# Kernel tuning notes

Measured on AMD Instinct MI355X. Metric: run time of the kernel, lower is better.

The kernel has to match this reference:

```python
import jax, jax.numpy as jnp
import numpy as np

DEPTH = 10
NUM_LEAVES = 2 ** DEPTH  # 1024


def setup_inputs() -> dict:
    key = jax.random.key(0)
    k1, k2, k3, k4 = jax.random.split(key, 4)
    B, C, T = 4096, 512, 4096
    x = jax.random.normal(k1, (B, C), dtype=jnp.float32)
    # thresholds = 6*rand - 3, as in __init__
    thresholds = 6.0 * jax.random.uniform(k2, (T, NUM_LEAVES - 1), dtype=jnp.float32) - 3.0
    ordinals = jax.random.randint(k3, (T, NUM_LEAVES - 1), 0, C, dtype=jnp.int32)
    weights = jax.random.normal(k4, (T, NUM_LEAVES), dtype=jnp.float32)
    return {"x": x, "thresholds": thresholds, "ordinals": ordinals, "weights": weights}


def reference(x, thresholds, ordinals, weights):
    """Random hinge forest forward.

    For each sample b and tree t: traverse the perfect binary tree of depth
    DEPTH.  At node n, margin m = x[b, ordinals[t, n]] - thresholds[t, n];
    go right (child 2n+2) if m > 0 else left (child 2n+1).  Track the signed
    margin of minimum magnitude along the path.  Output is
    |min-margin| * weights[t, leaf].
    """
    B = x.shape[0]
    T = thresholds.shape[0]
    tr = jnp.arange(T)  # [T], broadcasts against [B, T] node indices
    node = jnp.zeros((B, T), dtype=jnp.int32)
    minm = jnp.full((B, T), jnp.inf, dtype=x.dtype)
    for _ in range(DEPTH):
        thr = thresholds[tr, node]                      # [B, T]
        ordv = ordinals[tr, node]                       # [B, T] feature ids
        feat = jnp.take_along_axis(x, ordv, axis=1)     # [B, T]
        m = feat - thr
        minm = jnp.where(jnp.abs(m) < jnp.abs(minm), m, minm)
        node = 2 * node + 1 + (m > 0).astype(jnp.int32)
    leaf = node - (NUM_LEAVES - 1)                      # [B, T] in [0, 2^depth)
    w = weights[tr, leaf]                               # [B, T]
    return jnp.abs(minm) * w
```

## Files before the change

kernel.cpp:

```cpp
#include <hip/hip_runtime.h>
#include <hip/hip_fp16.h>

#define BB 4096
#define CC 512
#define TT 4096
#define NN 1023
#define NL 1024


__device__ __forceinline__ unsigned pack_node(float th, int o) {
    return ((unsigned)o << 16) | (unsigned)__half_as_ushort(__float2half(th));
}

__global__ __launch_bounds__(256)
void pack_trees(const float* __restrict__ thr, const int* __restrict__ ord,
                const float* __restrict__ wts, unsigned* __restrict__ pk_lo,
                uint2* __restrict__ p8, uint4* __restrict__ tails) {
    int t = blockIdx.x, tid = threadIdx.x;
    const float* tr = thr + (size_t)t * NN;
    const int*   oo = ord + (size_t)t * NN;
    unsigned* plo = pk_lo + ((size_t)t << 8);
    plo[tid] = (tid == 0) ? 0u : pack_node(tr[tid - 1], oo[tid - 1]);
    if (tid < 128) {
        int j = tid;
        p8[((size_t)t << 7) + j] =
            make_uint2(pack_node(tr[255 + 2 * j], oo[255 + 2 * j]),
                       pack_node(tr[256 + 2 * j], oo[256 + 2 * j]));
    }
    int i = tid;
    int nL = 511 + 2 * i, nR = 512 + 2 * i;
    unsigned ndL = pack_node(tr[nL], oo[nL]);
    unsigned ndR = pack_node(tr[nR], oo[nR]);
    float4 w4 = *(const float4*)(wts + ((size_t)t << 10) + 4 * i);
    unsigned w01 = (unsigned)__half_as_ushort(__float2half(w4.x)) |
                   ((unsigned)__half_as_ushort(__float2half(w4.y)) << 16);
    unsigned w23 = (unsigned)__half_as_ushort(__float2half(w4.z)) |
                   ((unsigned)__half_as_ushort(__float2half(w4.w)) << 16);
    tails[((size_t)t << 8) + i] = make_uint4(ndL, ndR, w01, w23);
}

__global__ __launch_bounds__(256)
void pack_x16(const float* __restrict__ x, unsigned short* __restrict__ xt16) {
    __shared__ float tile[64][65];
    int tx = threadIdx.x & 63, ty = threadIdx.x >> 6;
    int b0 = blockIdx.x * 64;
    int c0 = blockIdx.y * 64;
    #pragma unroll
    for (int i = 0; i < 16; ++i) {
        int rr = i * 4 + ty;
        tile[rr][tx] = x[(size_t)(b0 + rr) * CC + c0 + tx];
    }
    __syncthreads();
    #pragma unroll
    for (int i = 0; i < 16; ++i) {
        int cr = i * 4 + ty;
        xt16[(size_t)(c0 + cr) * BB + b0 + tx] =
            __half_as_ushort(__float2half(tile[tx][cr]));
    }
}

typedef unsigned short u16x2 __attribute__((ext_vector_type(2)));

static __device__ __forceinline__ unsigned psub_f16x2(unsigned a, unsigned b) {
    __half2 ah, bh;
    __builtin_memcpy(&ah, &a, 4);
    __builtin_memcpy(&bh, &b, 4);
    __half2 r = ah - bh;
    unsigned u; __builtin_memcpy(&u, &r, 4); return u;
}
static __device__ __forceinline__ unsigned pmin_u16x2(unsigned a, unsigned b) {
    u16x2 av, bv;
    __builtin_memcpy(&av, &a, 4);
    __builtin_memcpy(&bv, &b, 4);
    u16x2 m = __builtin_elementwise_min(av, bv);
    unsigned u; __builtin_memcpy(&u, &m, 4); return u;
}
static __device__ __forceinline__ float f16lo(unsigned u) {
    return __half2float(__ushort_as_half((unsigned short)(u & 0xffffu)));
}
static __device__ __forceinline__ float f16hi(unsigned u) {
    return __half2float(__ushort_as_half((unsigned short)(u >> 16)));
}

#define LDS_BYTES 163840

typedef __attribute__((address_space(1))) const void gv_t;
typedef __attribute__((address_space(3))) void lv_t;

__global__ __launch_bounds__(1024, 1)
void rhf_main(const unsigned* __restrict__ pk_lo, const uint2* __restrict__ p8g,
              const uint4* __restrict__ tails, const unsigned short* __restrict__ xt16,
              float* __restrict__ out) {
    extern __shared__ char smem[];
    unsigned short* xs16 = (unsigned short*)smem;
    unsigned*       trl  = (unsigned*)(smem + 65536);
    float*          res  = (float*)(smem + 131072);

    const int tid  = threadIdx.x;
    const int lane = tid & 63;
    const int wv   = tid >> 6;
    const int bi   = blockIdx.x;
    const int tb    = ((bi & 7) << 2) + ((bi >> 3) >> 6);
    const int panel = (bi >> 3) & 63;

    const char* gsrc0 = (const char*)pk_lo + ((size_t)(tb * 128) << 10);
    char* ldst = (char*)trl + wv * 4096 + lane * 16;
    auto dma = [&](int g) {
        const char* s = gsrc0 + ((size_t)(g * 64 + wv * 4) << 10) + lane * 16;
        #pragma unroll
        for (int q = 0; q < 4; ++q)
            __builtin_amdgcn_global_load_lds((gv_t*)(s + q * 1024),
                                             (lv_t*)(ldst + q * 1024), 16, 0, 0);
    };

    dma(0);

    {
        const unsigned short* src = xt16 + (size_t)panel * 64;
        #pragma unroll
        for (int k = 0; k < 4; ++k) {
            int i4 = k * 1024 + tid;
            int c  = i4 >> 3;
            int o8 = (i4 & 7) << 3;
            uint4 v = *(const uint4*)(src + (size_t)c * BB + o8);
            *(uint4*)(xs16 + ((size_t)i4 << 3)) = v;
        }
    }
    __syncthreads();

    auto evalpair = [&](unsigned nd_a, unsigned nd_b, unsigned& amin,
                        unsigned& r_a, unsigned& r_b) {
        unsigned thv2 = (nd_a & 0xffffu) | (nd_b << 16);
        unsigned short fa = xs16[((nd_a >> 16) << 6) + lane];
        unsigned short fb = xs16[((nd_b >> 16) << 6) + lane];
        unsigned feat2 = (unsigned)fa | ((unsigned)fb << 16);
        unsigned mb = psub_f16x2(feat2, thv2);
        amin = pmin_u16x2(amin, mb & 0x7fff7fffu);
        r_a = ((mb >> 15) & 1u) ^ 1u;
        r_b = (mb >> 31) ^ 1u;
    };

    #pragma unroll 1
    for (int g = 0; g < 2; ++g) {
        if (g > 0) {
            asm volatile("s_waitcnt vmcnt(0)" ::: "memory");
            __builtin_amdgcn_sched_barrier(0);
        }
        const int t0 = tb * 128 + g * 64 + wv * 4;
        const unsigned* pkw = trl + wv * 1024;

        unsigned amin01 = 0x7c007c00u, amin23 = 0x7c007c00u;
        int sl0 = 1, sl1 = 1, sl2 = 1, sl3 = 1;
        unsigned nd0 = pkw[1], nd1 = pkw[256 + 1], nd2 = pkw[512 + 1], nd3 = pkw[768 + 1];

        #pragma unroll
        for (int d = 0; d < 7; ++d) {
            uint2 ch0 = *(const uint2*)(pkw +       2 * sl0);
            uint2 ch1 = *(const uint2*)(pkw + 256 + 2 * sl1);
            uint2 ch2 = *(const uint2*)(pkw + 512 + 2 * sl2);
            uint2 ch3 = *(const uint2*)(pkw + 768 + 2 * sl3);
            unsigned r0, r1, r2, r3;
            evalpair(nd0, nd1, amin01, r0, r1);
            evalpair(nd2, nd3, amin23, r2, r3);
            sl0 = 2 * sl0 + (int)r0; nd0 = r0 ? ch0.y : ch0.x;
            sl1 = 2 * sl1 + (int)r1; nd1 = r1 ? ch1.y : ch1.x;
            sl2 = 2 * sl2 + (int)r2; nd2 = r2 ? ch2.y : ch2.x;
            sl3 = 2 * sl3 + (int)r3; nd3 = r3 ? ch3.y : ch3.x;
        }

        const uint2* p8t = p8g + ((size_t)t0 << 7);
        uint2 q0 = p8t[        sl0 - 128];
        uint2 q1 = p8t[128 +   sl1 - 128];
        uint2 q2 = p8t[256 +   sl2 - 128];
        uint2 q3 = p8t[384 +   sl3 - 128];
        {
            unsigned r0, r1, r2, r3;
            evalpair(nd0, nd1, amin01, r0, r1);
            evalpair(nd2, nd3, amin23, r2, r3);
            sl0 = 2 * sl0 + (int)r0; nd0 = r0 ? q0.y : q0.x;
            sl1 = 2 * sl1 + (int)r1; nd1 = r1 ? q1.y : q1.x;
            sl2 = 2 * sl2 + (int)r2; nd2 = r2 ? q2.y : q2.x;
            sl3 = 2 * sl3 + (int)r3; nd3 = r3 ? q3.y : q3.x;
        }

        const uint4* tt = tails + ((size_t)t0 << 8);
        uint4 e0 = tt[        sl0 - 256];
        uint4 e1 = tt[256 +   sl1 - 256];
        uint4 e2 = tt[512 +   sl2 - 256];
        uint4 e3 = tt[768 +   sl3 - 256];
        if (g == 0) { dma(1); __builtin_amdgcn_sched_barrier(0); }
        unsigned w0, w1, w2, w3;
        {
            unsigned r0, r1, r2, r3;
            evalpair(nd0, nd1, amin01, r0, r1);
            evalpair(nd2, nd3, amin23, r2, r3);
            nd0 = r0 ? e0.y : e0.x;  w0 = r0 ? e0.w : e0.z;
            nd1 = r1 ? e1.y : e1.x;  w1 = r1 ? e1.w : e1.z;
            nd2 = r2 ? e2.y : e2.x;  w2 = r2 ? e2.w : e2.z;
            nd3 = r3 ? e3.y : e3.x;  w3 = r3 ? e3.w : e3.z;
        }

        {
            unsigned r0, r1, r2, r3;
            evalpair(nd0, nd1, amin01, r0, r1);
            evalpair(nd2, nd3, amin23, r2, r3);
            unsigned short wb0 = (unsigned short)(r0 ? (w0 >> 16) : (w0 & 0xffffu));
            unsigned short wb1 = (unsigned short)(r1 ? (w1 >> 16) : (w1 & 0xffffu));
            unsigned short wb2 = (unsigned short)(r2 ? (w2 >> 16) : (w2 & 0xffffu));
            unsigned short wb3 = (unsigned short)(r3 ? (w3 >> 16) : (w3 & 0xffffu));
            float o0 = f16lo(amin01) * __half2float(__ushort_as_half(wb0));
            float o1 = f16hi(amin01) * __half2float(__ushort_as_half(wb1));
            float o2 = f16lo(amin23) * __half2float(__ushort_as_half(wb2));
            float o3 = f16hi(amin23) * __half2float(__ushort_as_half(wb3));
            int col0 = g * 64 + wv * 4;
            res[(lane << 7) + ((col0 +     lane) & 127)] = o0;
            res[(lane << 7) + ((col0 + 1 + lane) & 127)] = o1;
            res[(lane << 7) + ((col0 + 2 + lane) & 127)] = o2;
            res[(lane << 7) + ((col0 + 3 + lane) & 127)] = o3;
        }
    }
    __syncthreads();

    float* obase = out + (size_t)(tb * 128);
    #pragma unroll
    for (int k = 0; k < 8; ++k) {
        int idx = k * 1024 + tid;
        int rr = idx >> 7, cc = idx & 127;
        float v = res[(rr << 7) + ((cc + rr) & 127)];
        obase[((size_t)panel * 64 + rr) * TT + cc] = v;
    }
}

#define F_SP 32
#define F_TG 16
#define F_GROUPS 8
#define F_TPB (F_TG * F_GROUPS)
#define F_NPANELS (BB / F_SP)
#define F_LDS 147456

__global__ __launch_bounds__(512, 1)
void rhf_fallback(const float* __restrict__ x, const float* __restrict__ thr_g,
                  const int* __restrict__ ord_g, const float* __restrict__ wts,
                  float* __restrict__ out) {
    extern __shared__ char smem[];
    float*        xs  = (float*)(smem);
    unsigned int* pk  = (unsigned int*)(smem + 65536);
    float*        res = (float*)(smem + 131072);
    const int tid = threadIdx.x, s = tid & 31, slot = tid >> 5;
    const int panel = blockIdx.x & (F_NPANELS - 1), tb = blockIdx.x >> 7;
    const float* xbase = x + (size_t)panel * F_SP * CC;
    #pragma unroll
    for (int k = 0; k < (F_SP * CC) / 512; ++k) {
        int idx = k * 512 + tid, r = idx >> 9, c = idx & 511;
        xs[(c << 5) + r] = xbase[r * CC + c];
    }
    float4 pthr[8]; int4 pord[8]; float tthr[3]; int tord[3];
    auto prefetch = [&](int g) {
        const size_t base = (size_t)(tb * F_TPB + g * F_TG + slot) * NN;
        #pragma unroll
        for (int k = 0; k < 8; ++k) {
            int j = k * 128 + 4 * s;
            if (j < 1020) { pthr[k] = *(const float4*)(thr_g + base + j);
                            pord[k] = *(const int4*)(ord_g + base + j); }
            else { tthr[0]=thr_g[base+1020]; tord[0]=ord_g[base+1020];
                   tthr[1]=thr_g[base+1021]; tord[1]=ord_g[base+1021];
                   tthr[2]=thr_g[base+1022]; tord[2]=ord_g[base+1022]; }
        }
    };
    auto pack1 = [](float f, int o) -> unsigned int {
        return ((unsigned int)o << 16) | (unsigned int)__half_as_ushort(__float2half(f));
    };
    auto commit = [&]() {
        unsigned int* pt = pk + (slot << 10);
        #pragma unroll
        for (int k = 0; k < 8; ++k) {
            int j = k * 128 + 4 * s;
            if (j < 1020) {
                pt[1+j+0]=pack1(pthr[k].x,pord[k].x); pt[1+j+1]=pack1(pthr[k].y,pord[k].y);
                pt[1+j+2]=pack1(pthr[k].z,pord[k].z); pt[1+j+3]=pack1(pthr[k].w,pord[k].w);
            } else { pt[1+1020]=pack1(tthr[0],tord[0]); pt[1+1021]=pack1(tthr[1],tord[1]);
                     pt[1+1022]=pack1(tthr[2],tord[2]); }
        }
    };
    prefetch(0);
    __builtin_amdgcn_sched_barrier(0);
    for (int g = 0; g < F_GROUPS; ++g) {
        __syncthreads();
        commit();
        __syncthreads();
        if (g + 1 < F_GROUPS) prefetch(g + 1);
        __builtin_amdgcn_sched_barrier(0);
        const int t = tb * F_TPB + g * F_TG + slot;
        const unsigned int* pkt = pk + (slot << 10);
        float minm = __builtin_inff();
        int sl = 1;
        unsigned int cur = pkt[1];
        #pragma unroll
        for (int d = 0; d < 10; ++d) {
            uint2 ch;
            if (d < 9) ch = *(const uint2*)(pkt + 2 * sl);
            float thv = __half2float(__ushort_as_half((unsigned short)(cur & 0xffffu)));
            int orv = (int)(cur >> 16);
            float feat = xs[(orv << 5) + s];
            float m = feat - thv;
            bool take = fabsf(m) < fabsf(minm);
            minm = take ? m : minm;
            int right = (m > 0.0f) ? 1 : 0;
            sl = 2 * sl + right;
            if (d < 9) cur = right ? ch.y : ch.x;
        }
        int leaf = sl - NL;
        float w = wts[(size_t)t * NL + leaf];
        int col = g * F_TG + slot;
        res[(s << 7) + ((col + s) & 127)] = fabsf(minm) * w;
    }
    __syncthreads();
    float* obase = out + (size_t)panel * F_SP * TT + (size_t)tb * F_TPB;
    #pragma unroll
    for (int k = 0; k < (F_SP * F_TPB) / 512; ++k) {
        int idx = k * 512 + tid, rr = idx >> 7, c = idx & 127;
        obase[(size_t)rr * TT + c] = res[(rr << 7) + ((c + rr) & 127)];
    }
}

extern "C" void kernel_launch(void* const* d_in, const int* in_sizes, int n_in,
                              void* d_out, int out_size, void* d_ws, size_t ws_size,
                              hipStream_t stream) {
    const float* x    = (const float*)d_in[0];
    const float* thr  = (const float*)d_in[1];
    const int*   ordv = (const int*)d_in[2];
    const float* wts  = (const float*)d_in[3];
    float*       out  = (float*)d_out;

    const size_t pk_bytes   = (size_t)TT * 256 * 4;
    const size_t p8_bytes   = (size_t)TT * 128 * 8;
    const size_t tail_bytes = (size_t)TT * 256 * 16;
    const size_t xt_bytes   = (size_t)CC * BB * 2;

    if (d_ws && ws_size >= pk_bytes + p8_bytes + tail_bytes + xt_bytes) {
        unsigned*       pk_lo = (unsigned*)d_ws;
        uint2*          p8    = (uint2*)((char*)d_ws + pk_bytes);
        uint4*          tails = (uint4*)((char*)d_ws + pk_bytes + p8_bytes);
        unsigned short* xt16  = (unsigned short*)((char*)d_ws + pk_bytes + p8_bytes + tail_bytes);
        pack_trees<<<TT, 256, 0, stream>>>(thr, ordv, wts, pk_lo, p8, tails);
        dim3 gx(BB / 64, CC / 64);
        pack_x16<<<gx, 256, 0, stream>>>(x, xt16);
        (void)hipFuncSetAttribute((const void*)rhf_main,
                            hipFuncAttributeMaxDynamicSharedMemorySize, LDS_BYTES);
        rhf_main<<<2048, 1024, LDS_BYTES, stream>>>(pk_lo, p8, tails, xt16, out);
    } else {
        (void)hipFuncSetAttribute((const void*)rhf_fallback,
                            hipFuncAttributeMaxDynamicSharedMemorySize, F_LDS);
        rhf_fallback<<<F_NPANELS * (TT / F_TPB), 512, F_LDS, stream>>>(x, thr, ordv, wts, out);
    }
}
```

Baseline: 114.6 us.

## Stage only top seven tree levels in LDS and interleave eight trees per wave

Only the first 7 levels of each tree (128 nodes) are now staged in LDS, so all 128 trees of a block fit in one load and the two-pass loop with its mid-kernel DMA disappears. Level 7 moves to a new global g7 array. Each wave now traverses 8 trees at once instead of 4, giving more independent loads in flight. The ordinal is pre-shifted by 23 so it becomes a byte offset into the x tile, removing a shift per lookup. In exchange, one more dependent global gather is added per sample, and register pressure rises with the wider interleave.

```diff
diff --git a/kernel.cpp b/kernel.cpp
--- a/kernel.cpp
+++ b/kernel.cpp
@@ -9,21 +9,30 @@
 
 
 __device__ __forceinline__ unsigned pack_node(float th, int o) {
-    return ((unsigned)o << 16) | (unsigned)__half_as_ushort(__float2half(th));
+    return ((unsigned)o << 23) | (unsigned)__half_as_ushort(__float2half(th));
 }
 
 __global__ __launch_bounds__(256)
 void pack_trees(const float* __restrict__ thr, const int* __restrict__ ord,
                 const float* __restrict__ wts, unsigned* __restrict__ pk_lo,
-                uint2* __restrict__ p8, uint4* __restrict__ tails) {
+                uint2* __restrict__ g7, uint2* __restrict__ g8,
+                uint4* __restrict__ tails) {
     int t = blockIdx.x, tid = threadIdx.x;
     const float* tr = thr + (size_t)t * NN;
     const int*   oo = ord + (size_t)t * NN;
-    unsigned* plo = pk_lo + ((size_t)t << 8);
-    plo[tid] = (tid == 0) ? 0u : pack_node(tr[tid - 1], oo[tid - 1]);
+    if (tid < 128) {
+        unsigned* plo = pk_lo + ((size_t)t << 7);
+        plo[tid] = (tid == 0) ? 0u : pack_node(tr[tid - 1], oo[tid - 1]);
+    }
+    if (tid < 64) {
+        int j = tid;
+        g7[((size_t)t << 6) + j] =
+            make_uint2(pack_node(tr[127 + 2 * j], oo[127 + 2 * j]),
+                       pack_node(tr[128 + 2 * j], oo[128 + 2 * j]));
+    }
     if (tid < 128) {
         int j = tid;
-        p8[((size_t)t << 7) + j] =
+        g8[((size_t)t << 7) + j] =
             make_uint2(pack_node(tr[255 + 2 * j], oo[255 + 2 * j]),
                        pack_node(tr[256 + 2 * j], oo[256 + 2 * j]));
     }
@@ -88,13 +97,13 @@
 typedef __attribute__((address_space(3))) void lv_t;
 
 __global__ __launch_bounds__(1024, 1)
-void rhf_main(const unsigned* __restrict__ pk_lo, const uint2* __restrict__ p8g,
-              const uint4* __restrict__ tails, const unsigned short* __restrict__ xt16,
-              float* __restrict__ out) {
+void rhf_main(const unsigned* __restrict__ pk_lo, const uint2* __restrict__ g7g,
+              const uint2* __restrict__ g8g, const uint4* __restrict__ tails,
+              const unsigned short* __restrict__ xt16, float* __restrict__ out) {
     extern __shared__ char smem[];
-    unsigned short* xs16 = (unsigned short*)smem;
-    unsigned*       trl  = (unsigned*)(smem + 65536);
-    float*          res  = (float*)(smem + 131072);
+    const char*     xsb = (const char*)smem;
+    unsigned*       trl = (unsigned*)(smem + 65536);
+    float*          res = (float*)(smem + 131072);
 
     const int tid  = threadIdx.x;
     const int lane = tid & 63;
@@ -102,18 +111,16 @@
     const int bi   = blockIdx.x;
     const int tb    = ((bi & 7) << 2) + ((bi >> 3) >> 6);
     const int panel = (bi >> 3) & 63;
-
-    const char* gsrc0 = (const char*)pk_lo + ((size_t)(tb * 128) << 10);
-    char* ldst = (char*)trl + wv * 4096 + lane * 16;
-    auto dma = [&](int g) {
-        const char* s = gsrc0 + ((size_t)(g * 64 + wv * 4) << 10) + lane * 16;
+    const int lane2 = lane << 1;
+
+    {
+        const char* s = (const char*)pk_lo + ((size_t)(tb * 128 + wv * 8) << 9) + lane * 16;
+        char* d = (char*)trl + wv * 4096 + lane * 16;
         #pragma unroll
         for (int q = 0; q < 4; ++q)
             __builtin_amdgcn_global_load_lds((gv_t*)(s + q * 1024),
-                                             (lv_t*)(ldst + q * 1024), 16, 0, 0);
-    };
-
-    dma(0);
+                                             (lv_t*)(d + q * 1024), 16, 0, 0);
+    }
 
     {
         const unsigned short* src = xt16 + (size_t)panel * 64;
@@ -123,16 +130,19 @@
             int c  = i4 >> 3;
             int o8 = (i4 & 7) << 3;
             uint4 v = *(const uint4*)(src + (size_t)c * BB + o8);
-            *(uint4*)(xs16 + ((size_t)i4 << 3)) = v;
+            *(uint4*)((char*)smem + ((size_t)i4 << 4)) = v;
         }
     }
     __syncthreads();
+
+    const int t0 = tb * 128 + wv * 8;
+    const unsigned* pkw = trl + wv * 1024;
 
     auto evalpair = [&](unsigned nd_a, unsigned nd_b, unsigned& amin,
                         unsigned& r_a, unsigned& r_b) {
         unsigned thv2 = (nd_a & 0xffffu) | (nd_b << 16);
-        unsigned short fa = xs16[((nd_a >> 16) << 6) + lane];
-        unsigned short fb = xs16[((nd_b >> 16) << 6) + lane];
+        unsigned short fa = *(const unsigned short*)(xsb + (nd_a >> 16) + lane2);
+        unsigned short fb = *(const unsigned short*)(xsb + (nd_b >> 16) + lane2);
         unsigned feat2 = (unsigned)fa | ((unsigned)fb << 16);
         unsigned mb = psub_f16x2(feat2, thv2);
         amin = pmin_u16x2(amin, mb & 0x7fff7fffu);
@@ -140,83 +150,88 @@
         r_b = (mb >> 31) ^ 1u;
     };
 
-    #pragma unroll 1
-    for (int g = 0; g < 2; ++g) {
-        if (g > 0) {
-            asm volatile("s_waitcnt vmcnt(0)" ::: "memory");
-            __builtin_amdgcn_sched_barrier(0);
-        }
-        const int t0 = tb * 128 + g * 64 + wv * 4;
-        const unsigned* pkw = trl + wv * 1024;
-
-        unsigned amin01 = 0x7c007c00u, amin23 = 0x7c007c00u;
-        int sl0 = 1, sl1 = 1, sl2 = 1, sl3 = 1;
-        unsigned nd0 = pkw[1], nd1 = pkw[256 + 1], nd2 = pkw[512 + 1], nd3 = pkw[768 + 1];
-
-        #pragma unroll
-        for (int d = 0; d < 7; ++d) {
-            uint2 ch0 = *(const uint2*)(pkw +       2 * sl0);
-            uint2 ch1 = *(const uint2*)(pkw + 256 + 2 * sl1);
-            uint2 ch2 = *(const uint2*)(pkw + 512 + 2 * sl2);
-            uint2 ch3 = *(const uint2*)(pkw + 768 + 2 * sl3);
-            unsigned r0, r1, r2, r3;
-            evalpair(nd0, nd1, amin01, r0, r1);
-            evalpair(nd2, nd3, amin23, r2, r3);
-            sl0 = 2 * sl0 + (int)r0; nd0 = r0 ? ch0.y : ch0.x;
-            sl1 = 2 * sl1 + (int)r1; nd1 = r1 ? ch1.y : ch1.x;
-            sl2 = 2 * sl2 + (int)r2; nd2 = r2 ? ch2.y : ch2.x;
-            sl3 = 2 * sl3 + (int)r3; nd3 = r3 ? ch3.y : ch3.x;
-        }
-
-        const uint2* p8t = p8g + ((size_t)t0 << 7);
-        uint2 q0 = p8t[        sl0 - 128];
-        uint2 q1 = p8t[128 +   sl1 - 128];
-        uint2 q2 = p8t[256 +   sl2 - 128];
-        uint2 q3 = p8t[384 +   sl3 - 128];
-        {
-            unsigned r0, r1, r2, r3;
-            evalpair(nd0, nd1, amin01, r0, r1);
-            evalpair(nd2, nd3, amin23, r2, r3);
-            sl0 = 2 * sl0 + (int)r0; nd0 = r0 ? q0.y : q0.x;
-            sl1 = 2 * sl1 + (int)r1; nd1 = r1 ? q1.y : q1.x;
-            sl2 = 2 * sl2 + (int)r2; nd2 = r2 ? q2.y : q2.x;
-            sl3 = 2 * sl3 + (int)r3; nd3 = r3 ? q3.y : q3.x;
-        }
-
-        const uint4* tt = tails + ((size_t)t0 << 8);
-        uint4 e0 = tt[        sl0 - 256];
-        uint4 e1 = tt[256 +   sl1 - 256];
-        uint4 e2 = tt[512 +   sl2 - 256];
-        uint4 e3 = tt[768 +   sl3 - 256];
-        if (g == 0) { dma(1); __builtin_amdgcn_sched_barrier(0); }
-        unsigned w0, w1, w2, w3;
-        {
-            unsigned r0, r1, r2, r3;
-            evalpair(nd0, nd1, amin01, r0, r1);
-            evalpair(nd2, nd3, amin23, r2, r3);
-            nd0 = r0 ? e0.y : e0.x;  w0 = r0 ? e0.w : e0.z;
-            nd1 = r1 ? e1.y : e1.x;  w1 = r1 ? e1.w : e1.z;
-            nd2 = r2 ? e2.y : e2.x;  w2 = r2 ? e2.w : e2.z;
-            nd3 = r3 ? e3.y : e3.x;  w3 = r3 ? e3.w : e3.z;
-        }
-
-        {
-            unsigned r0, r1, r2, r3;
-            evalpair(nd0, nd1, amin01, r0, r1);
-            evalpair(nd2, nd3, amin23, r2, r3);
-            unsigned short wb0 = (unsigned short)(r0 ? (w0 >> 16) : (w0 & 0xffffu));
-            unsigned short wb1 = (unsigned short)(r1 ? (w1 >> 16) : (w1 & 0xffffu));
-            unsigned short wb2 = (unsigned short)(r2 ? (w2 >> 16) : (w2 & 0xffffu));
-            unsigned short wb3 = (unsigned short)(r3 ? (w3 >> 16) : (w3 & 0xffffu));
-            float o0 = f16lo(amin01) * __half2float(__ushort_as_half(wb0));
-            float o1 = f16hi(amin01) * __half2float(__ushort_as_half(wb1));
-            float o2 = f16lo(amin23) * __half2float(__ushort_as_half(wb2));
-            float o3 = f16hi(amin23) * __half2float(__ushort_as_half(wb3));
-            int col0 = g * 64 + wv * 4;
-            res[(lane << 7) + ((col0 +     lane) & 127)] = o0;
-            res[(lane << 7) + ((col0 + 1 + lane) & 127)] = o1;
-            res[(lane << 7) + ((col0 + 2 + lane) & 127)] = o2;
-            res[(lane << 7) + ((col0 + 3 + lane) & 127)] = o3;
+    unsigned amin[4];
+    int      sl[8];
+    unsigned nd[8];
+    unsigned r[8];
+    #pragma unroll
+    for (int p = 0; p < 4; ++p) amin[p] = 0x7c007c00u;
+    #pragma unroll
+    for (int c = 0; c < 8; ++c) { sl[c] = 1; nd[c] = pkw[c * 128 + 1]; }
+
+    #pragma unroll
+    for (int d = 0; d < 6; ++d) {
+        uint2 ch[8];
+        #pragma unroll
+        for (int c = 0; c < 8; ++c)
+            ch[c] = *(const uint2*)(pkw + c * 128 + 2 * sl[c]);
+        #pragma unroll
+        for (int p = 0; p < 4; ++p)
+            evalpair(nd[2 * p], nd[2 * p + 1], amin[p], r[2 * p], r[2 * p + 1]);
+        #pragma unroll
+        for (int c = 0; c < 8; ++c) {
+            sl[c] = 2 * sl[c] + (int)r[c];
+            nd[c] = r[c] ? ch[c].y : ch[c].x;
+        }
+    }
+
+    {
+        uint2 q[8];
+        #pragma unroll
+        for (int c = 0; c < 8; ++c)
+            q[c] = g7g[((size_t)(t0 + c) << 6) + (sl[c] - 64)];
+        #pragma unroll
+        for (int p = 0; p < 4; ++p)
+            evalpair(nd[2 * p], nd[2 * p + 1], amin[p], r[2 * p], r[2 * p + 1]);
+        #pragma unroll
+        for (int c = 0; c < 8; ++c) {
+            sl[c] = 2 * sl[c] + (int)r[c];
+            nd[c] = r[c] ? q[c].y : q[c].x;
+        }
+    }
+
+    {
+        uint2 q[8];
+        #pragma unroll
+        for (int c = 0; c < 8; ++c)
+            q[c] = g8g[((size_t)(t0 + c) << 7) + (sl[c] - 128)];
+        #pragma unroll
+        for (int p = 0; p < 4; ++p)
+            evalpair(nd[2 * p], nd[2 * p + 1], amin[p], r[2 * p], r[2 * p + 1]);
+        #pragma unroll
+        for (int c = 0; c < 8; ++c) {
+            sl[c] = 2 * sl[c] + (int)r[c];
+            nd[c] = r[c] ? q[c].y : q[c].x;
+        }
+    }
+
+    unsigned wsel[8];
+    {
+        uint4 e[8];
+        #pragma unroll
+        for (int c = 0; c < 8; ++c)
+            e[c] = tails[((size_t)(t0 + c) << 8) + (sl[c] - 256)];
+        #pragma unroll
+        for (int p = 0; p < 4; ++p)
+            evalpair(nd[2 * p], nd[2 * p + 1], amin[p], r[2 * p], r[2 * p + 1]);
+        #pragma unroll
+        for (int c = 0; c < 8; ++c) {
+            nd[c]   = r[c] ? e[c].y : e[c].x;
+            wsel[c] = r[c] ? e[c].w : e[c].z;
+        }
+    }
+
+    {
+        #pragma unroll
+        for (int p = 0; p < 4; ++p)
+            evalpair(nd[2 * p], nd[2 * p + 1], amin[p], r[2 * p], r[2 * p + 1]);
+        #pragma unroll
+        for (int c = 0; c < 8; ++c) {
+            unsigned short wb = (unsigned short)(r[c] ? (wsel[c] >> 16) : (wsel[c] & 0xffffu));
+            float am = (c & 1) ? f16hi(amin[c >> 1]) : f16lo(amin[c >> 1]);
+            float o  = am * __half2float(__ushort_as_half(wb));
+            int col = wv * 8 + c;
+            res[(lane << 7) + ((col + lane) & 127)] = o;
         }
     }
     __syncthreads();
@@ -332,22 +347,25 @@
     const float* wts  = (const float*)d_in[3];
     float*       out  = (float*)d_out;
 
-    const size_t pk_bytes   = (size_t)TT * 256 * 4;
-    const size_t p8_bytes   = (size_t)TT * 128 * 8;
+    const size_t pk_bytes   = (size_t)TT * 128 * 4;
+    const size_t g7_bytes   = (size_t)TT * 64 * 8;
+    const size_t g8_bytes   = (size_t)TT * 128 * 8;
     const size_t tail_bytes = (size_t)TT * 256 * 16;
     const size_t xt_bytes   = (size_t)CC * BB * 2;
 
-    if (d_ws && ws_size >= pk_bytes + p8_bytes + tail_bytes + xt_bytes) {
-        unsigned*       pk_lo = (unsigned*)d_ws;
-        uint2*          p8    = (uint2*)((char*)d_ws + pk_bytes);
-        uint4*          tails = (uint4*)((char*)d_ws + pk_bytes + p8_bytes);
-        unsigned short* xt16  = (unsigned short*)((char*)d_ws + pk_bytes + p8_bytes + tail_bytes);
-        pack_trees<<<TT, 256, 0, stream>>>(thr, ordv, wts, pk_lo, p8, tails);
+    if (d_ws && ws_size >= pk_bytes + g7_bytes + g8_bytes + tail_bytes + xt_bytes) {
+        char* p = (char*)d_ws;
+        unsigned*       pk_lo = (unsigned*)p;            p += pk_bytes;
+        uint2*          g7    = (uint2*)p;               p += g7_bytes;
+        uint2*          g8    = (uint2*)p;               p += g8_bytes;
+        uint4*          tails = (uint4*)p;               p += tail_bytes;
+        unsigned short* xt16  = (unsigned short*)p;
+        pack_trees<<<TT, 256, 0, stream>>>(thr, ordv, wts, pk_lo, g7, g8, tails);
         dim3 gx(BB / 64, CC / 64);
         pack_x16<<<gx, 256, 0, stream>>>(x, xt16);
         (void)hipFuncSetAttribute((const void*)rhf_main,
                             hipFuncAttributeMaxDynamicSharedMemorySize, LDS_BYTES);
-        rhf_main<<<2048, 1024, LDS_BYTES, stream>>>(pk_lo, p8, tails, xt16, out);
+        rhf_main<<<2048, 1024, LDS_BYTES, stream>>>(pk_lo, g7, g8, tails, xt16, out);
     } else {
         (void)hipFuncSetAttribute((const void*)rhf_fallback,
                             hipFuncAttributeMaxDynamicSharedMemorySize, F_LDS);
```

New measurement: 111.6 us (median of 2 runs). 1.03x faster.
